# Optimization experiments

Measured on AMD Instinct MI355X. Metric: run time of the kernel, lower is better.

Reference implementation:

```python
import jax, jax.numpy as jnp
import numpy as np

DIM = 512
HEADS = 8
DIM_HEAD = 64
INNER = HEADS * DIM_HEAD  # 512
B, N = 4, 2048


def setup_inputs() -> dict:
    key = jax.random.key(0)
    k1, k2, k3, k4 = jax.random.split(key, 4)
    x = jax.random.normal(k1, (B, N, DIM), dtype=jnp.float32)
    # nn.Linear(dim, inner*3, bias=False): weight [3*inner, dim]; store transposed [dim, 3*inner]
    w_qkv = jax.random.normal(k2, (DIM, 3 * INNER), dtype=jnp.float32) / np.sqrt(DIM)
    w_out = jax.random.normal(k3, (INNER, DIM), dtype=jnp.float32) / np.sqrt(INNER)
    b_out = jax.random.normal(k4, (DIM,), dtype=jnp.float32) * 0.01
    return {"x": x, "w_qkv": w_qkv, "w_out": w_out, "b_out": b_out}


def reference(x, w_qkv, w_out, b_out):
    b, n, _ = x.shape
    scale = DIM_HEAD ** -0.5
    qkv = x @ w_qkv  # [b, n, 3*inner]
    q, k, v = jnp.split(qkv, 3, axis=-1)
    # [b, n, h, d] -> [b, h, n, d]
    reshape = lambda t: t.reshape(b, n, HEADS, DIM_HEAD).transpose(0, 2, 1, 3)
    q, k, v = reshape(q), reshape(k), reshape(v)
    dots = jnp.einsum('bhid,bhjd->bhij', q, k) * scale  # [b, h, n, n]
    attn = jax.nn.softmax(dots, axis=-1)
    out = jnp.einsum('bhij,bhjd->bhid', attn, v)  # [b, h, n, d]
    out = out.transpose(0, 2, 1, 3).reshape(b, n, INNER)
    return out @ w_out + b_out  # dropout is identity at inference
```

## Files before the change

### kernel.cpp

```cpp
#include <hip/hip_runtime.h>
#include <hip/hip_bf16.h>
#include <cstdint>

#define DEV __device__ __forceinline__

typedef __attribute__((ext_vector_type(8))) __bf16 bf16x8;
typedef __attribute__((ext_vector_type(4))) float floatx4;
typedef __attribute__((ext_vector_type(4))) short shortx4;
typedef __attribute__((ext_vector_type(8))) short shortx8;

constexpr float QSCALE = 0.18033688011112042f;

DEV unsigned short f2b(float f) {
  union { float f; unsigned u; } v; v.f = f;
  return (unsigned short)((v.u + 0x7fffu + ((v.u >> 16) & 1u)) >> 16);
}

#if defined(__has_builtin) && __has_builtin(__builtin_amdgcn_cvt_pk_bf16_f32)
DEV unsigned pk2(float a, float b) {
  typedef __attribute__((ext_vector_type(2))) __bf16 bf2;
  union { bf2 v; unsigned u; } u;
  u.v = __builtin_amdgcn_cvt_pk_bf16_f32(a, b);
  return u.u;
}
#else
DEV unsigned pk2(float a, float b) {
  return (unsigned)f2b(a) | ((unsigned)f2b(b) << 16);
}
#endif

#if defined(__has_builtin) && __has_builtin(__builtin_amdgcn_exp2f)
DEV float fexp2(float x) { return __builtin_amdgcn_exp2f(x); }
#else
DEV float fexp2(float x) { return exp2f(x); }
#endif

DEV floatx4 mfma16(bf16x8 a, bf16x8 b, floatx4 c) {
  return __builtin_amdgcn_mfma_f32_16x16x32_bf16(a, b, c, 0, 0, 0);
}

#define GLD_LDS16(gp, lp)                                                          \
  __builtin_amdgcn_global_load_lds(                                                \
      (const __attribute__((address_space(1))) void*)(gp),                         \
      (__attribute__((address_space(3))) void*)(lp), 16, 0, 0)

__global__ void cvt_f32_bf16(const float* __restrict__ in,
                             unsigned short* __restrict__ out, int n4) {
  int i = blockIdx.x * 256 + threadIdx.x;
  if (i >= n4) return;
  floatx4 f = ((const floatx4*)in)[i];
  shortx4 s;
  s[0] = (short)f2b(f[0]); s[1] = (short)f2b(f[1]);
  s[2] = (short)f2b(f[2]); s[3] = (short)f2b(f[3]);
  ((shortx4*)out)[i] = s;
}

__global__ void tcvt(const float* __restrict__ in, unsigned short* __restrict__ out,
                     int R, int C) {
  __shared__ float tile[32][33];
  int tx = threadIdx.x & 31, ty = threadIdx.x >> 5;
  int r0 = blockIdx.y * 32, c0 = blockIdx.x * 32;
#pragma unroll
  for (int i = 0; i < 4; i++) {
    int rr = ty + i * 8;
    tile[rr][tx] = in[(size_t)(r0 + rr) * C + c0 + tx];
  }
  __syncthreads();
#pragma unroll
  for (int i = 0; i < 4; i++) {
    int rr = ty + i * 8;
    out[(size_t)(c0 + rr) * R + r0 + tx] = f2b(tile[tx][rr]);
  }
}

__global__ __launch_bounds__(256, 2) void gemm_qkv(
    const unsigned short* __restrict__ A, const unsigned short* __restrict__ Bt,
    unsigned short* __restrict__ qg, unsigned short* __restrict__ kg,
    unsigned short* __restrict__ vtg) {
  __shared__ __align__(16) unsigned short smem[24576];
  const int tid = threadIdx.x;
  const int lane = tid & 63, wid = tid >> 6;
  const int g = lane >> 4, r = lane & 15;
  const int m0 = blockIdx.y * 256, n0 = blockIdx.x * 128;
  const int wm = (wid & 1) * 128, wn = (wid >> 1) * 64;
  const int K = 512;

  floatx4 acc[8][4] = {};

  int rowA[4], kbA[4];
#pragma unroll
  for (int i = 0; i < 4; i++) {
    int c = i * 256 + tid;
    rowA[i] = c >> 2;
    kbA[i] = (c & 3) ^ ((rowA[i] >> 1) & 3);
  }

#define STAGE_QKV(kt, b)                                                         \
  {                                                                              \
    _Pragma("unroll") for (int i = 0; i < 4; i++)                                \
        GLD_LDS16(A + (size_t)(m0 + rowA[i]) * K + (kt) + kbA[i] * 8,            \
                  (char*)smem + (b)*16384 + i * 4096 + wid * 1024);              \
    _Pragma("unroll") for (int i = 0; i < 2; i++)                                \
        GLD_LDS16(Bt + (size_t)(n0 + rowA[i]) * K + (kt) + kbA[i] * 8,           \
                  (char*)smem + 32768 + (b)*8192 + i * 4096 + wid * 1024);       \
  }

  STAGE_QKV(0, 0)
  for (int it = 0; it < 16; it++) {
    const int buf = it & 1;
    __syncthreads();
    if (it + 1 < 16) STAGE_QKV((it + 1) * 32, buf ^ 1)
    const unsigned short* Xs = smem + buf * 8192;
    const unsigned short* Ws = smem + 16384 + buf * 4096;
    bf16x8 a[8], b[4];
#pragma unroll
    for (int t = 0; t < 8; t++) {
      int rw = wm + t * 16 + r;
      a[t] = *(const bf16x8*)(Xs + rw * 32 + (g ^ ((rw >> 1) & 3)) * 8);
    }
#pragma unroll
    for (int t = 0; t < 4; t++) {
      int rw = wn + t * 16 + r;
      b[t] = *(const bf16x8*)(Ws + rw * 32 + (g ^ ((rw >> 1) & 3)) * 8);
    }
#pragma unroll
    for (int mt = 0; mt < 8; mt++)
#pragma unroll
      for (int nt = 0; nt < 4; nt++)
        acc[mt][nt] = mfma16(a[mt], b[nt], acc[mt][nt]);
  }
#undef STAGE_QKV

  const int which = blockIdx.x >> 2;
  if (which == 2) {
    const int tokbase = m0 + wm;
    const int bb = tokbase >> 11, nbase = tokbase & 2047;
#pragma unroll
    for (int mt = 0; mt < 8; mt++) {
      const int m3 = mt & 3;
      const int s = (mt >> 2) * 64 + (m3 >> 1) * 32 + g * 8 + (m3 & 1) * 4;
#pragma unroll
      for (int nt = 0; nt < 4; nt++) {
        int vcol = n0 + wn + nt * 16 + r - 1024;
        int h = vcol >> 6, d = vcol & 63;
        unsigned long long w =
            (unsigned long long)pk2(acc[mt][nt][0], acc[mt][nt][1]) |
            ((unsigned long long)pk2(acc[mt][nt][2], acc[mt][nt][3]) << 32);
        *(unsigned long long*)(vtg + ((size_t)(bb * 8 + h) * 64 + d) * 2048 +
                               nbase + s) = w;
      }
    }
  } else {
    const float sc = (which == 0) ? QSCALE : 1.f;
    unsigned short* dst = (which == 0) ? qg : kg;
#pragma unroll
    for (int half = 0; half < 2; half++) {
      __syncthreads();
      if ((wid & 1) == half) {
#pragma unroll
        for (int mt = 0; mt < 8; mt++)
#pragma unroll
          for (int nt = 0; nt < 4; nt++) {
            int rl = mt * 16 + g * 4;
            int col = wn + nt * 16 + r;
#pragma unroll
            for (int e = 0; e < 4; e++)
              smem[(rl + e) * 136 + col] = f2b(acc[mt][nt][e] * sc);
          }
      }
      __syncthreads();
#pragma unroll
      for (int it = 0; it < 8; it++) {
        int c = it * 256 + tid;
        int row = c >> 4, cc = c & 15;
        shortx8 v = *(const shortx8*)(smem + row * 136 + cc * 8);
        int gq = n0 + cc * 8;
        int h = (gq >> 6) & 7, d0 = gq & 63;
        int tok = m0 + half * 128 + row, bb = tok >> 11, n = tok & 2047;
        *(shortx8*)(dst + ((size_t)(bb * 8 + h) * 2048 + n) * 64 + d0) = v;
      }
    }
  }
}

__global__ __launch_bounds__(256, 2) void gemm_out(
    const unsigned short* __restrict__ A, const unsigned short* __restrict__ Bt,
    float* __restrict__ outF, const float* __restrict__ bias) {
  __shared__ __align__(16) unsigned short smem[17408];
  const int tid = threadIdx.x;
  const int lane = tid & 63, wid = tid >> 6;
  const int g = lane >> 4, r = lane & 15;
  const int m0 = blockIdx.y * 128, n0 = blockIdx.x * 128;
  const int wm = (wid & 1) * 64, wn = (wid >> 1) * 64;
  const int K = 512;

  floatx4 acc[4][4] = {};

  int rowA[2], kbA[2];
#pragma unroll
  for (int i = 0; i < 2; i++) {
    int c = i * 256 + tid;
    rowA[i] = c >> 2;
    kbA[i] = (c & 3) ^ ((rowA[i] >> 1) & 3);
  }

#define STAGE_OUT(kt, b)                                                         \
  {                                                                              \
    _Pragma("unroll") for (int i = 0; i < 2; i++) {                              \
      GLD_LDS16(A + (size_t)(m0 + rowA[i]) * K + (kt) + kbA[i] * 8,              \
                (char*)smem + (b)*8192 + i * 4096 + wid * 1024);                 \
      GLD_LDS16(Bt + (size_t)(n0 + rowA[i]) * K + (kt) + kbA[i] * 8,             \
                (char*)smem + 16384 + (b)*8192 + i * 4096 + wid * 1024);         \
    }                                                                            \
  }

  STAGE_OUT(0, 0)
  for (int it = 0; it < 16; it++) {
    const int buf = it & 1;
    __syncthreads();
    if (it + 1 < 16) STAGE_OUT((it + 1) * 32, buf ^ 1)
    const unsigned short* Xs = smem + buf * 4096;
    const unsigned short* Ws = smem + 8192 + buf * 4096;
    bf16x8 a[4], b[4];
#pragma unroll
    for (int t = 0; t < 4; t++) {
      int rw = wm + t * 16 + r;
      a[t] = *(const bf16x8*)(Xs + rw * 32 + (g ^ ((rw >> 1) & 3)) * 8);
      int rb = wn + t * 16 + r;
      b[t] = *(const bf16x8*)(Ws + rb * 32 + (g ^ ((rb >> 1) & 3)) * 8);
    }
#pragma unroll
    for (int mt = 0; mt < 4; mt++)
#pragma unroll
      for (int nt = 0; nt < 4; nt++)
        acc[mt][nt] = mfma16(a[mt], b[nt], acc[mt][nt]);
  }
#undef STAGE_OUT

  float* ftile = (float*)smem;
#pragma unroll
  for (int half = 0; half < 2; half++) {
    __syncthreads();
#pragma unroll
    for (int mi = 0; mi < 2; mi++) {
      int mt = half * 2 + mi;
#pragma unroll
      for (int nt = 0; nt < 4; nt++)
#pragma unroll
        for (int e = 0; e < 4; e++) {
          int lr = (wm >> 1) + mi * 16 + g * 4 + e;
          ftile[lr * 132 + wn + nt * 16 + r] = acc[mt][nt][e];
        }
    }
    __syncthreads();
#pragma unroll
    for (int it = 0; it < 8; it++) {
      int c = it * 256 + tid;
      int lr = c >> 5, cc = c & 31;
      floatx4 v = *(const floatx4*)(ftile + lr * 132 + cc * 4);
      int col = n0 + cc * 4;
      v += *(const floatx4*)(bias + col);
      int rowt = (lr < 32) ? (half * 32 + lr) : (64 + half * 32 + (lr - 32));
      *(floatx4*)(outF + (size_t)(m0 + rowt) * 512 + col) = v;
    }
  }
}

__global__ __launch_bounds__(256, 2) void attn(
    const unsigned short* __restrict__ qg, const unsigned short* __restrict__ kg,
    const unsigned short* __restrict__ vtg, unsigned short* __restrict__ ao) {
  __shared__ __align__(16) char L[65536];
  unsigned short* Ksm = (unsigned short*)L;
  unsigned short* Vtm = (unsigned short*)(L + 32768);
  const int tid = threadIdx.x, lane = tid & 63, wid = tid >> 6;
  const int g = lane >> 4, r = lane & 15, r7 = r & 7;
  const int wq = wid & 1, wk = wid >> 1;
  const int bh = blockIdx.y;
  const int q0 = blockIdx.x * 128 + wq * 64;
  const size_t base = (size_t)bh * (2048 * 64);
  const int chunk = (lane & 7) ^ ((lane >> 3) & 7);
  const int srow = lane >> 3;

  bf16x8 bq[4][2];
#pragma unroll
  for (int nt = 0; nt < 4; nt++)
#pragma unroll
    for (int kc = 0; kc < 2; kc++)
      bq[nt][kc] = *(const bf16x8*)(qg + base + (size_t)(q0 + nt * 16 + r) * 64 +
                                    kc * 32 + g * 8);

  bf16x8 vones;
#pragma unroll
  for (int i = 0; i < 8; i++) vones[i] = (__bf16)1.0f;

  floatx4 o[4][4] = {};
  floatx4 lacc[4] = {};

#define STAGE_ATTN(it, b)                                                        \
  {                                                                              \
    const int sn0 = (it)*128 + wk * 64;                                          \
    if (wq == 0) {                                                               \
      _Pragma("unroll") for (int j = 0; j < 8; j++)                              \
          GLD_LDS16(kg + base + (size_t)(sn0 + j * 8 + srow) * 64 + chunk * 8,   \
                    (char*)L + ((b)*2 + wk) * 8192 + j * 1024);                  \
    } else {                                                                     \
      _Pragma("unroll") for (int j = 0; j < 8; j++)                              \
          GLD_LDS16(vtg + base + (size_t)(j * 8 + srow) * 2048 + sn0 + chunk * 8,\
                    (char*)L + 32768 + ((b)*2 + wk) * 8192 + j * 1024);          \
    }                                                                            \
  }

  STAGE_ATTN(0, 0)
  for (int it = 0; it < 16; it++) {
    const int buf = it & 1;
    __syncthreads();
    if (it + 1 < 16) STAGE_ATTN(it + 1, buf ^ 1)
    const unsigned short* Kt = Ksm + (buf * 2 + wk) * 4096;
    const unsigned short* Vt = Vtm + (buf * 2 + wk) * 4096;

    floatx4 st[4][4] = {};
#pragma unroll
    for (int kc = 0; kc < 2; kc++)
#pragma unroll
      for (int mt = 0; mt < 4; mt++) {
        bf16x8 ak = *(const bf16x8*)(Kt + (mt * 16 + r) * 64 +
                                     ((kc * 4 + g) ^ r7) * 8);
#pragma unroll
        for (int nt = 0; nt < 4; nt++)
          st[mt][nt] = mfma16(ak, bq[nt][kc], st[mt][nt]);
      }

    bf16x8 ap[4][2];
#pragma unroll
    for (int a = 0; a < 4; a++) {
      float p[4][4];
#pragma unroll
      for (int mt = 0; mt < 4; mt++)
#pragma unroll
        for (int e = 0; e < 4; e++) p[mt][e] = fexp2(st[mt][a][e]);
#pragma unroll
      for (int kc = 0; kc < 2; kc++) {
        union { unsigned u[4]; bf16x8 v; } w;
        w.u[0] = pk2(p[2 * kc][0], p[2 * kc][1]);
        w.u[1] = pk2(p[2 * kc][2], p[2 * kc][3]);
        w.u[2] = pk2(p[2 * kc + 1][0], p[2 * kc + 1][1]);
        w.u[3] = pk2(p[2 * kc + 1][2], p[2 * kc + 1][3]);
        ap[a][kc] = w.v;
      }
    }

#pragma unroll
    for (int kc = 0; kc < 2; kc++) {
      bf16x8 bv[4];
#pragma unroll
      for (int b = 0; b < 4; b++)
        bv[b] = *(const bf16x8*)(Vt + (b * 16 + r) * 64 +
                                 ((kc * 4 + g) ^ r7) * 8);
#pragma unroll
      for (int a = 0; a < 4; a++) {
        lacc[a] = mfma16(ap[a][kc], vones, lacc[a]);
#pragma unroll
        for (int b = 0; b < 4; b++)
          o[a][b] = mfma16(ap[a][kc], bv[b], o[a][b]);
      }
    }
  }
#undef STAGE_ATTN

  float* fP = (float*)L;
  float* fL = (float*)(L + 32768);
  unsigned short* Osm = (unsigned short*)(L + 40960);
  __syncthreads();
  if (wk == 1) {
#pragma unroll
    for (int a = 0; a < 4; a++) {
      *(floatx4*)&fL[wq * 1024 + a * 256 + lane * 4] = lacc[a];
#pragma unroll
      for (int b = 0; b < 4; b++)
        *(floatx4*)&fP[wq * 4096 + (a * 4 + b) * 256 + lane * 4] = o[a][b];
    }
  }
  __syncthreads();
  if (wk == 0) {
#pragma unroll
    for (int a = 0; a < 4; a++) {
      floatx4 lt = lacc[a] + *(floatx4*)&fL[wq * 1024 + a * 256 + lane * 4];
      floatx4 il;
#pragma unroll
      for (int e = 0; e < 4; e++) il[e] = 1.f / lt[e];
#pragma unroll
      for (int b = 0; b < 4; b++) {
        floatx4 oo = o[a][b] +
                     *(floatx4*)&fP[wq * 4096 + (a * 4 + b) * 256 + lane * 4];
#pragma unroll
        for (int e = 0; e < 4; e++)
          Osm[wq * 4608 + (a * 16 + g * 4 + e) * 72 + b * 16 + r] =
              f2b(oo[e] * il[e]);
      }
    }
  }
  __syncthreads();
  const int bb = bh >> 3, h = bh & 7;
#pragma unroll
  for (int it = 0; it < 4; it++) {
    int c = it * 256 + tid;
    int row = c >> 3, cc = c & 7;
    int wqi = row >> 6, r6 = row & 63;
    shortx8 v = *(const shortx8*)(Osm + wqi * 4608 + r6 * 72 + cc * 8);
    int tok = blockIdx.x * 128 + row;
    *(shortx8*)(ao + ((size_t)(bb * 2048 + tok)) * 512 + h * 64 + cc * 8) = v;
  }
}

extern "C" void kernel_launch(void* const* d_in, const int* in_sizes, int n_in,
                              void* d_out, int out_size, void* d_ws, size_t ws_size,
                              hipStream_t stream) {
  const float* x = (const float*)d_in[0];
  const float* w_qkv = (const float*)d_in[1];
  const float* w_out = (const float*)d_in[2];
  const float* b_out = (const float*)d_in[3];
  float* out = (float*)d_out;

  unsigned short* wsp = (unsigned short*)d_ws;
  unsigned short* xb = wsp;
  unsigned short* wqkvt = xb + (size_t)8192 * 512;
  unsigned short* woutt = wqkvt + (size_t)1536 * 512;
  unsigned short* qg = woutt + (size_t)512 * 512;
  unsigned short* kg = qg + (size_t)32 * 2048 * 64;
  unsigned short* vtg = kg + (size_t)32 * 2048 * 64;
  unsigned short* ao = vtg + (size_t)32 * 2048 * 64;

  cvt_f32_bf16<<<4096, 256, 0, stream>>>(x, xb, 8192 * 512 / 4);
  tcvt<<<dim3(48, 16), 256, 0, stream>>>(w_qkv, wqkvt, 512, 1536);
  tcvt<<<dim3(16, 16), 256, 0, stream>>>(w_out, woutt, 512, 512);
  gemm_qkv<<<dim3(12, 32), 256, 0, stream>>>(xb, wqkvt, qg, kg, vtg);
  attn<<<dim3(16, 32), 256, 0, stream>>>(qg, kg, vtg, ao);
  gemm_out<<<dim3(4, 64), 256, 0, stream>>>(ao, woutt, out, b_out);
}
```

Measured before the change: 157.7 us.

## Store Q/K/V in MFMA fragment order and stream attention operands from global into registers

The QKV GEMM now writes Q, K and V in a fragment-major layout that matches the MFMA operand order, so the attention kernel can load K and V straight from global memory into registers, double-buffered in software, instead of staging them through LDS with barriers. The QKV GEMM moves to 128x128 tiles with higher occupancy, the output GEMM uses smaller 64-row tiles to launch more blocks, and the two weight-transpose launches are merged into one. The aim is to remove LDS traffic and syncthreads from the attention inner loop and cut launch overhead. The cost is that every K/V load now hits global memory or L2 directly, which raises register pressure and makes the kernel more sensitive to memory latency.

```diff
diff --git a/kernel.cpp b/kernel.cpp
--- a/kernel.cpp
+++ b/kernel.cpp
@@ -55,11 +55,17 @@
   ((shortx4*)out)[i] = s;
 }
 
-__global__ void tcvt(const float* __restrict__ in, unsigned short* __restrict__ out,
-                     int R, int C) {
+__global__ void tcvt2(const float* __restrict__ w_qkv,
+                      const float* __restrict__ w_out,
+                      unsigned short* __restrict__ wqkvt,
+                      unsigned short* __restrict__ woutt) {
   __shared__ float tile[32][33];
+  const float* in; unsigned short* out; int C, bx;
+  if (blockIdx.x < 48) { in = w_qkv; out = wqkvt; C = 1536; bx = blockIdx.x; }
+  else { in = w_out; out = woutt; C = 512; bx = blockIdx.x - 48; }
+  const int R = 512;
   int tx = threadIdx.x & 31, ty = threadIdx.x >> 5;
-  int r0 = blockIdx.y * 32, c0 = blockIdx.x * 32;
+  int r0 = blockIdx.y * 32, c0 = bx * 32;
 #pragma unroll
   for (int i = 0; i < 4; i++) {
     int rr = ty + i * 8;
@@ -73,119 +79,10 @@
   }
 }
 
-__global__ __launch_bounds__(256, 2) void gemm_qkv(
+__global__ __launch_bounds__(256, 3) void gemm_qkv(
     const unsigned short* __restrict__ A, const unsigned short* __restrict__ Bt,
-    unsigned short* __restrict__ qg, unsigned short* __restrict__ kg,
-    unsigned short* __restrict__ vtg) {
-  __shared__ __align__(16) unsigned short smem[24576];
-  const int tid = threadIdx.x;
-  const int lane = tid & 63, wid = tid >> 6;
-  const int g = lane >> 4, r = lane & 15;
-  const int m0 = blockIdx.y * 256, n0 = blockIdx.x * 128;
-  const int wm = (wid & 1) * 128, wn = (wid >> 1) * 64;
-  const int K = 512;
-
-  floatx4 acc[8][4] = {};
-
-  int rowA[4], kbA[4];
-#pragma unroll
-  for (int i = 0; i < 4; i++) {
-    int c = i * 256 + tid;
-    rowA[i] = c >> 2;
-    kbA[i] = (c & 3) ^ ((rowA[i] >> 1) & 3);
-  }
-
-#define STAGE_QKV(kt, b)                                                         \
-  {                                                                              \
-    _Pragma("unroll") for (int i = 0; i < 4; i++)                                \
-        GLD_LDS16(A + (size_t)(m0 + rowA[i]) * K + (kt) + kbA[i] * 8,            \
-                  (char*)smem + (b)*16384 + i * 4096 + wid * 1024);              \
-    _Pragma("unroll") for (int i = 0; i < 2; i++)                                \
-        GLD_LDS16(Bt + (size_t)(n0 + rowA[i]) * K + (kt) + kbA[i] * 8,           \
-                  (char*)smem + 32768 + (b)*8192 + i * 4096 + wid * 1024);       \
-  }
-
-  STAGE_QKV(0, 0)
-  for (int it = 0; it < 16; it++) {
-    const int buf = it & 1;
-    __syncthreads();
-    if (it + 1 < 16) STAGE_QKV((it + 1) * 32, buf ^ 1)
-    const unsigned short* Xs = smem + buf * 8192;
-    const unsigned short* Ws = smem + 16384 + buf * 4096;
-    bf16x8 a[8], b[4];
-#pragma unroll
-    for (int t = 0; t < 8; t++) {
-      int rw = wm + t * 16 + r;
-      a[t] = *(const bf16x8*)(Xs + rw * 32 + (g ^ ((rw >> 1) & 3)) * 8);
-    }
-#pragma unroll
-    for (int t = 0; t < 4; t++) {
-      int rw = wn + t * 16 + r;
-      b[t] = *(const bf16x8*)(Ws + rw * 32 + (g ^ ((rw >> 1) & 3)) * 8);
-    }
-#pragma unroll
-    for (int mt = 0; mt < 8; mt++)
-#pragma unroll
-      for (int nt = 0; nt < 4; nt++)
-        acc[mt][nt] = mfma16(a[mt], b[nt], acc[mt][nt]);
-  }
-#undef STAGE_QKV
-
-  const int which = blockIdx.x >> 2;
-  if (which == 2) {
-    const int tokbase = m0 + wm;
-    const int bb = tokbase >> 11, nbase = tokbase & 2047;
-#pragma unroll
-    for (int mt = 0; mt < 8; mt++) {
-      const int m3 = mt & 3;
-      const int s = (mt >> 2) * 64 + (m3 >> 1) * 32 + g * 8 + (m3 & 1) * 4;
-#pragma unroll
-      for (int nt = 0; nt < 4; nt++) {
-        int vcol = n0 + wn + nt * 16 + r - 1024;
-        int h = vcol >> 6, d = vcol & 63;
-        unsigned long long w =
-            (unsigned long long)pk2(acc[mt][nt][0], acc[mt][nt][1]) |
-            ((unsigned long long)pk2(acc[mt][nt][2], acc[mt][nt][3]) << 32);
-        *(unsigned long long*)(vtg + ((size_t)(bb * 8 + h) * 64 + d) * 2048 +
-                               nbase + s) = w;
-      }
-    }
-  } else {
-    const float sc = (which == 0) ? QSCALE : 1.f;
-    unsigned short* dst = (which == 0) ? qg : kg;
-#pragma unroll
-    for (int half = 0; half < 2; half++) {
-      __syncthreads();
-      if ((wid & 1) == half) {
-#pragma unroll
-        for (int mt = 0; mt < 8; mt++)
-#pragma unroll
-          for (int nt = 0; nt < 4; nt++) {
-            int rl = mt * 16 + g * 4;
-            int col = wn + nt * 16 + r;
-#pragma unroll
-            for (int e = 0; e < 4; e++)
-              smem[(rl + e) * 136 + col] = f2b(acc[mt][nt][e] * sc);
-          }
-      }
-      __syncthreads();
-#pragma unroll
-      for (int it = 0; it < 8; it++) {
-        int c = it * 256 + tid;
-        int row = c >> 4, cc = c & 15;
-        shortx8 v = *(const shortx8*)(smem + row * 136 + cc * 8);
-        int gq = n0 + cc * 8;
-        int h = (gq >> 6) & 7, d0 = gq & 63;
-        int tok = m0 + half * 128 + row, bb = tok >> 11, n = tok & 2047;
-        *(shortx8*)(dst + ((size_t)(bb * 8 + h) * 2048 + n) * 64 + d0) = v;
-      }
-    }
-  }
-}
-
-__global__ __launch_bounds__(256, 2) void gemm_out(
-    const unsigned short* __restrict__ A, const unsigned short* __restrict__ Bt,
-    float* __restrict__ outF, const float* __restrict__ bias) {
+    unsigned short* __restrict__ qf, unsigned short* __restrict__ kf,
+    unsigned short* __restrict__ vf) {
   __shared__ __align__(16) unsigned short smem[17408];
   const int tid = threadIdx.x;
   const int lane = tid & 63, wid = tid >> 6;
@@ -204,7 +101,7 @@
     kbA[i] = (c & 3) ^ ((rowA[i] >> 1) & 3);
   }
 
-#define STAGE_OUT(kt, b)                                                         \
+#define STAGE_G(kt, b)                                                           \
   {                                                                              \
     _Pragma("unroll") for (int i = 0; i < 2; i++) {                              \
       GLD_LDS16(A + (size_t)(m0 + rowA[i]) * K + (kt) + kbA[i] * 8,              \
@@ -214,11 +111,11 @@
     }                                                                            \
   }
 
-  STAGE_OUT(0, 0)
+  STAGE_G(0, 0)
   for (int it = 0; it < 16; it++) {
     const int buf = it & 1;
     __syncthreads();
-    if (it + 1 < 16) STAGE_OUT((it + 1) * 32, buf ^ 1)
+    if (it + 1 < 16) STAGE_G((it + 1) * 32, buf ^ 1)
     const unsigned short* Xs = smem + buf * 4096;
     const unsigned short* Ws = smem + 8192 + buf * 4096;
     bf16x8 a[4], b[4];
@@ -235,137 +132,215 @@
       for (int nt = 0; nt < 4; nt++)
         acc[mt][nt] = mfma16(a[mt], b[nt], acc[mt][nt]);
   }
-#undef STAGE_OUT
-
-  float* ftile = (float*)smem;
-#pragma unroll
-  for (int half = 0; half < 2; half++) {
+#undef STAGE_G
+
+  const int which = blockIdx.x >> 2;
+  if (which == 2) {
+    const int tokbase = m0 + wm;
+    const int bb = tokbase >> 11, vt = (tokbase & 2047) >> 6;
+#pragma unroll
+    for (int nt = 0; nt < 4; nt++) {
+      int vcol = n0 + wn + nt * 16 + r - 1024;
+      int h = vcol >> 6;
+      size_t hb = (size_t)(bb * 8 + h) * 131072 + (size_t)vt * 4096 + nt * 1024 +
+                  (g * 16 + r) * 8;
+#pragma unroll
+      for (int kc = 0; kc < 2; kc++) {
+        union { unsigned u[4]; shortx8 v; } w;
+        w.u[0] = pk2(acc[2 * kc][nt][0], acc[2 * kc][nt][1]);
+        w.u[1] = pk2(acc[2 * kc][nt][2], acc[2 * kc][nt][3]);
+        w.u[2] = pk2(acc[2 * kc + 1][nt][0], acc[2 * kc + 1][nt][1]);
+        w.u[3] = pk2(acc[2 * kc + 1][nt][2], acc[2 * kc + 1][nt][3]);
+        *(shortx8*)(vf + hb + kc * 512) = w.v;
+      }
+    }
+  } else {
+    const float sc = (which == 0) ? QSCALE : 1.f;
+    unsigned short* dst = (which == 0) ? qf : kf;
     __syncthreads();
 #pragma unroll
-    for (int mi = 0; mi < 2; mi++) {
-      int mt = half * 2 + mi;
-#pragma unroll
-      for (int nt = 0; nt < 4; nt++)
-#pragma unroll
-        for (int e = 0; e < 4; e++) {
-          int lr = (wm >> 1) + mi * 16 + g * 4 + e;
-          ftile[lr * 132 + wn + nt * 16 + r] = acc[mt][nt][e];
-        }
-    }
+    for (int mt = 0; mt < 4; mt++)
+#pragma unroll
+      for (int nt = 0; nt < 4; nt++) {
+        int col = wn + nt * 16 + r;
+#pragma unroll
+        for (int e = 0; e < 4; e++)
+          smem[(wm + mt * 16 + g * 4 + e) * 136 + col] = f2b(acc[mt][nt][e] * sc);
+      }
     __syncthreads();
 #pragma unroll
     for (int it = 0; it < 8; it++) {
       int c = it * 256 + tid;
-      int lr = c >> 5, cc = c & 31;
-      floatx4 v = *(const floatx4*)(ftile + lr * 132 + cc * 4);
-      int col = n0 + cc * 4;
-      v += *(const floatx4*)(bias + col);
-      int rowt = (lr < 32) ? (half * 32 + lr) : (64 + half * 32 + (lr - 32));
-      *(floatx4*)(outF + (size_t)(m0 + rowt) * 512 + col) = v;
-    }
-  }
-}
-
-__global__ __launch_bounds__(256, 2) void attn(
-    const unsigned short* __restrict__ qg, const unsigned short* __restrict__ kg,
-    const unsigned short* __restrict__ vtg, unsigned short* __restrict__ ao) {
-  __shared__ __align__(16) char L[65536];
-  unsigned short* Ksm = (unsigned short*)L;
-  unsigned short* Vtm = (unsigned short*)(L + 32768);
-  const int tid = threadIdx.x, lane = tid & 63, wid = tid >> 6;
-  const int g = lane >> 4, r = lane & 15, r7 = r & 7;
-  const int wq = wid & 1, wk = wid >> 1;
-  const int bh = blockIdx.y;
-  const int q0 = blockIdx.x * 128 + wq * 64;
-  const size_t base = (size_t)bh * (2048 * 64);
-  const int chunk = (lane & 7) ^ ((lane >> 3) & 7);
-  const int srow = lane >> 3;
-
-  bf16x8 bq[4][2];
-#pragma unroll
-  for (int nt = 0; nt < 4; nt++)
-#pragma unroll
-    for (int kc = 0; kc < 2; kc++)
-      bq[nt][kc] = *(const bf16x8*)(qg + base + (size_t)(q0 + nt * 16 + r) * 64 +
-                                    kc * 32 + g * 8);
-
-  bf16x8 vones;
-#pragma unroll
-  for (int i = 0; i < 8; i++) vones[i] = (__bf16)1.0f;
-
-  floatx4 o[4][4] = {};
-  floatx4 lacc[4] = {};
-
-#define STAGE_ATTN(it, b)                                                        \
+      int row = c >> 4, cc = c & 15;
+      shortx8 v = *(const shortx8*)(smem + row * 136 + cc * 8);
+      int gq = n0 + cc * 8;
+      int h = (gq >> 6) & 7, d0 = gq & 63;
+      int kc = d0 >> 5, gp = (d0 >> 3) & 3;
+      int tok = m0 + row, bb = tok >> 11, n = tok & 2047;
+      *(shortx8*)(dst + (size_t)(bb * 8 + h) * 131072 + (n >> 4) * 1024 +
+                  kc * 512 + (gp * 16 + (n & 15)) * 8) = v;
+    }
+  }
+}
+
+__global__ __launch_bounds__(256, 2) void gemm_out(
+    const unsigned short* __restrict__ A, const unsigned short* __restrict__ Bt,
+    float* __restrict__ outF, const float* __restrict__ bias) {
+  __shared__ __align__(16) unsigned short smem[16896];
+  const int tid = threadIdx.x;
+  const int lane = tid & 63, wid = tid >> 6;
+  const int g = lane >> 4, r = lane & 15;
+  const int m0 = blockIdx.y * 64, n0 = blockIdx.x * 128;
+  const int wn = wid * 32;
+  const int K = 512;
+
+  floatx4 acc[4][2] = {};
+
+  const int rA = tid >> 2, kA = (tid & 3) ^ ((rA >> 1) & 3);
+  int rB[2], kB[2];
+#pragma unroll
+  for (int i = 0; i < 2; i++) {
+    int c = i * 256 + tid;
+    rB[i] = c >> 2;
+    kB[i] = (c & 3) ^ ((rB[i] >> 1) & 3);
+  }
+
+#define STAGE_O(kt, b)                                                           \
   {                                                                              \
-    const int sn0 = (it)*128 + wk * 64;                                          \
-    if (wq == 0) {                                                               \
-      _Pragma("unroll") for (int j = 0; j < 8; j++)                              \
-          GLD_LDS16(kg + base + (size_t)(sn0 + j * 8 + srow) * 64 + chunk * 8,   \
-                    (char*)L + ((b)*2 + wk) * 8192 + j * 1024);                  \
-    } else {                                                                     \
-      _Pragma("unroll") for (int j = 0; j < 8; j++)                              \
-          GLD_LDS16(vtg + base + (size_t)(j * 8 + srow) * 2048 + sn0 + chunk * 8,\
-                    (char*)L + 32768 + ((b)*2 + wk) * 8192 + j * 1024);          \
-    }                                                                            \
-  }
-
-  STAGE_ATTN(0, 0)
+    GLD_LDS16(A + (size_t)(m0 + rA) * K + (kt) + kA * 8,                         \
+              (char*)smem + (b)*4096 + wid * 1024);                              \
+    _Pragma("unroll") for (int i = 0; i < 2; i++)                                \
+        GLD_LDS16(Bt + (size_t)(n0 + rB[i]) * K + (kt) + kB[i] * 8,              \
+                  (char*)smem + 8192 + (b)*8192 + i * 4096 + wid * 1024);        \
+  }
+
+  STAGE_O(0, 0)
   for (int it = 0; it < 16; it++) {
     const int buf = it & 1;
     __syncthreads();
-    if (it + 1 < 16) STAGE_ATTN(it + 1, buf ^ 1)
-    const unsigned short* Kt = Ksm + (buf * 2 + wk) * 4096;
-    const unsigned short* Vt = Vtm + (buf * 2 + wk) * 4096;
-
-    floatx4 st[4][4] = {};
+    if (it + 1 < 16) STAGE_O((it + 1) * 32, buf ^ 1)
+    const unsigned short* Xs = smem + buf * 2048;
+    const unsigned short* Ws = smem + 4096 + buf * 4096;
+    bf16x8 a[4], b[2];
+#pragma unroll
+    for (int t = 0; t < 4; t++) {
+      int rw = t * 16 + r;
+      a[t] = *(const bf16x8*)(Xs + rw * 32 + (g ^ ((rw >> 1) & 3)) * 8);
+    }
+#pragma unroll
+    for (int t = 0; t < 2; t++) {
+      int rb = wn + t * 16 + r;
+      b[t] = *(const bf16x8*)(Ws + rb * 32 + (g ^ ((rb >> 1) & 3)) * 8);
+    }
+#pragma unroll
+    for (int mt = 0; mt < 4; mt++)
+#pragma unroll
+      for (int bt = 0; bt < 2; bt++)
+        acc[mt][bt] = mfma16(a[mt], b[bt], acc[mt][bt]);
+  }
+#undef STAGE_O
+
+  float* ftile = (float*)smem;
+  __syncthreads();
+#pragma unroll
+  for (int mt = 0; mt < 4; mt++)
+#pragma unroll
+    for (int bt = 0; bt < 2; bt++)
+#pragma unroll
+      for (int e = 0; e < 4; e++)
+        ftile[(mt * 16 + g * 4 + e) * 132 + wn + bt * 16 + r] = acc[mt][bt][e];
+  __syncthreads();
+#pragma unroll
+  for (int it = 0; it < 8; it++) {
+    int c = it * 256 + tid;
+    int lr = c >> 5, cc = c & 31;
+    floatx4 v = *(const floatx4*)(ftile + lr * 132 + cc * 4);
+    int col = n0 + cc * 4;
+    v += *(const floatx4*)(bias + col);
+    *(floatx4*)(outF + (size_t)(m0 + lr) * 512 + col) = v;
+  }
+}
+
+__global__ __launch_bounds__(256, 2) void attn(
+    const unsigned short* __restrict__ qf, const unsigned short* __restrict__ kf,
+    const unsigned short* __restrict__ vf, unsigned short* __restrict__ ao) {
+  __shared__ __align__(16) char L[59392];
+  const int tid = threadIdx.x, lane = tid & 63, wid = tid >> 6;
+  const int g = lane >> 4, r = lane & 15;
+  const int wq = wid & 1, wk = wid >> 1;
+  const int bh = blockIdx.y;
+  const size_t base = (size_t)bh * 131072;
+  const unsigned short* kb = kf + base;
+  const unsigned short* vb = vf + base;
+
+  const int qt0 = (blockIdx.x * 128 + wq * 64) >> 4;
+  bf16x8 bq[4][2];
+#pragma unroll
+  for (int nt = 0; nt < 4; nt++)
 #pragma unroll
     for (int kc = 0; kc < 2; kc++)
-#pragma unroll
-      for (int mt = 0; mt < 4; mt++) {
-        bf16x8 ak = *(const bf16x8*)(Kt + (mt * 16 + r) * 64 +
-                                     ((kc * 4 + g) ^ r7) * 8);
-#pragma unroll
-        for (int nt = 0; nt < 4; nt++)
-          st[mt][nt] = mfma16(ak, bq[nt][kc], st[mt][nt]);
-      }
-
-    bf16x8 ap[4][2];
-#pragma unroll
-    for (int a = 0; a < 4; a++) {
-      float p[4][4];
-#pragma unroll
-      for (int mt = 0; mt < 4; mt++)
-#pragma unroll
-        for (int e = 0; e < 4; e++) p[mt][e] = fexp2(st[mt][a][e]);
-#pragma unroll
-      for (int kc = 0; kc < 2; kc++) {
-        union { unsigned u[4]; bf16x8 v; } w;
-        w.u[0] = pk2(p[2 * kc][0], p[2 * kc][1]);
-        w.u[1] = pk2(p[2 * kc][2], p[2 * kc][3]);
-        w.u[2] = pk2(p[2 * kc + 1][0], p[2 * kc + 1][1]);
-        w.u[3] = pk2(p[2 * kc + 1][2], p[2 * kc + 1][3]);
-        ap[a][kc] = w.v;
-      }
-    }
-
-#pragma unroll
-    for (int kc = 0; kc < 2; kc++) {
-      bf16x8 bv[4];
-#pragma unroll
-      for (int b = 0; b < 4; b++)
-        bv[b] = *(const bf16x8*)(Vt + (b * 16 + r) * 64 +
-                                 ((kc * 4 + g) ^ r7) * 8);
-#pragma unroll
-      for (int a = 0; a < 4; a++) {
-        lacc[a] = mfma16(ap[a][kc], vones, lacc[a]);
-#pragma unroll
-        for (int b = 0; b < 4; b++)
-          o[a][b] = mfma16(ap[a][kc], bv[b], o[a][b]);
-      }
-    }
-  }
-#undef STAGE_ATTN
+      bq[nt][kc] = *(const bf16x8*)(qf + base + (size_t)(qt0 + nt) * 1024 +
+                                    kc * 512 + lane * 8);
+
+  bf16x8 vones;
+#pragma unroll
+  for (int i = 0; i < 8; i++) vones[i] = (__bf16)1.0f;
+
+  floatx4 o[4][4] = {};
+  floatx4 lacc[4] = {};
+
+#define LOADKV(akX, bvX, nn)                                                     \
+  {                                                                              \
+    _Pragma("unroll") for (int mt = 0; mt < 4; mt++)                             \
+      _Pragma("unroll") for (int kc = 0; kc < 2; kc++)                           \
+        akX[mt][kc] = *(const bf16x8*)(kb + (size_t)(nn)*64 + mt * 1024 +        \
+                                       kc * 512 + lane * 8);                     \
+    _Pragma("unroll") for (int b = 0; b < 4; b++)                                \
+      _Pragma("unroll") for (int kc = 0; kc < 2; kc++)                           \
+        bvX[b][kc] = *(const bf16x8*)(vb + (size_t)(nn)*64 + b * 1024 +          \
+                                      kc * 512 + lane * 8);                      \
+  }
+
+#define STEP(akC, bvC, akN, bvN, np, cond)                                       \
+  {                                                                              \
+    floatx4 st[4][4] = {};                                                       \
+    _Pragma("unroll") for (int kc = 0; kc < 2; kc++)                             \
+      _Pragma("unroll") for (int mt = 0; mt < 4; mt++)                           \
+        _Pragma("unroll") for (int nt = 0; nt < 4; nt++)                         \
+            st[mt][nt] = mfma16(akC[mt][kc], bq[nt][kc], st[mt][nt]);            \
+    if (cond) LOADKV(akN, bvN, np)                                               \
+    bf16x8 ap[4][2];                                                             \
+    _Pragma("unroll") for (int a = 0; a < 4; a++) {                              \
+      float p[4][4];                                                             \
+      _Pragma("unroll") for (int mt = 0; mt < 4; mt++)                           \
+        _Pragma("unroll") for (int e = 0; e < 4; e++)                            \
+            p[mt][e] = fexp2(st[mt][a][e]);                                      \
+      _Pragma("unroll") for (int kc = 0; kc < 2; kc++) {                         \
+        union { unsigned u[4]; bf16x8 v; } w;                                    \
+        w.u[0] = pk2(p[2 * kc][0], p[2 * kc][1]);                                \
+        w.u[1] = pk2(p[2 * kc][2], p[2 * kc][3]);                                \
+        w.u[2] = pk2(p[2 * kc + 1][0], p[2 * kc + 1][1]);                        \
+        w.u[3] = pk2(p[2 * kc + 1][2], p[2 * kc + 1][3]);                        \
+        ap[a][kc] = w.v;                                                         \
+      }                                                                          \
+    }                                                                            \
+    _Pragma("unroll") for (int kc = 0; kc < 2; kc++)                             \
+      _Pragma("unroll") for (int a = 0; a < 4; a++) {                            \
+        lacc[a] = mfma16(ap[a][kc], vones, lacc[a]);                             \
+        _Pragma("unroll") for (int b = 0; b < 4; b++)                            \
+            o[a][b] = mfma16(ap[a][kc], bvC[b][kc], o[a][b]);                    \
+      }                                                                          \
+  }
+
+  bf16x8 ak0[4][2], bv0[4][2], ak1[4][2], bv1[4][2];
+  LOADKV(ak0, bv0, wk * 64)
+  for (int it2 = 0; it2 < 8; it2++) {
+    const int na = it2 * 256 + wk * 64;
+    STEP(ak0, bv0, ak1, bv1, na + 128, true)
+    STEP(ak1, bv1, ak0, bv0, na + 256, it2 < 7)
+  }
+#undef STEP
+#undef LOADKV
 
   float* fP = (float*)L;
   float* fL = (float*)(L + 32768);
@@ -425,15 +400,14 @@
   unsigned short* xb = wsp;
   unsigned short* wqkvt = xb + (size_t)8192 * 512;
   unsigned short* woutt = wqkvt + (size_t)1536 * 512;
-  unsigned short* qg = woutt + (size_t)512 * 512;
-  unsigned short* kg = qg + (size_t)32 * 2048 * 64;
-  unsigned short* vtg = kg + (size_t)32 * 2048 * 64;
-  unsigned short* ao = vtg + (size_t)32 * 2048 * 64;
+  unsigned short* qf = woutt + (size_t)512 * 512;
+  unsigned short* kf = qf + (size_t)32 * 2048 * 64;
+  unsigned short* vf = kf + (size_t)32 * 2048 * 64;
+  unsigned short* ao = vf + (size_t)32 * 2048 * 64;
 
   cvt_f32_bf16<<<4096, 256, 0, stream>>>(x, xb, 8192 * 512 / 4);
-  tcvt<<<dim3(48, 16), 256, 0, stream>>>(w_qkv, wqkvt, 512, 1536);
-  tcvt<<<dim3(16, 16), 256, 0, stream>>>(w_out, woutt, 512, 512);
-  gemm_qkv<<<dim3(12, 32), 256, 0, stream>>>(xb, wqkvt, qg, kg, vtg);
-  attn<<<dim3(16, 32), 256, 0, stream>>>(qg, kg, vtg, ao);
-  gemm_out<<<dim3(4, 64), 256, 0, stream>>>(ao, woutt, out, b_out);
-}
+  tcvt2<<<dim3(64, 16), 256, 0, stream>>>(w_qkv, w_out, wqkvt, woutt);
+  gemm_qkv<<<dim3(12, 64), 256, 0, stream>>>(xb, wqkvt, qf, kf, vf);
+  attn<<<dim3(16, 32), 256, 0, stream>>>(qf, kf, vf, ao);
+  gemm_out<<<dim3(4, 128), 256, 0, stream>>>(ao, woutt, out, b_out);
+}
```

After: 179.8 us. 1.14x slower.
